# Performance work log

Measured on AMD Instinct MI355X. Metric: run time of the kernel, lower is better.

Reference implementation:

```python
import jax, jax.numpy as jnp
import numpy as np

BS, N, H = 8, 2048, 512
NEG_INF = -1.0e9
LEAKY_SLOPE = 0.01  # torch nn.LeakyReLU default


def setup_inputs() -> dict:
    key = jax.random.key(0)
    ks = jax.random.split(key, 8)
    feats = jax.random.normal(ks[0], (BS, N, H), dtype=jnp.float32)
    # random 0/1 adjacency with self-loops so every row has >=1 neighbor
    adj = jax.random.randint(ks[1], (BS, N, N), 0, 2).astype(jnp.float32)
    adj = jnp.maximum(adj, jnp.eye(N, dtype=jnp.float32)[None])
    s = 1.0 / np.sqrt(H)
    return {
        "feats": feats,
        "adj_mat": adj,
        "fc_w": jax.random.normal(ks[2], (H, H), dtype=jnp.float32) * s,
        "fc_b": jax.random.normal(ks[3], (H,), dtype=jnp.float32) * s,
        "q_w": jax.random.normal(ks[4], (1, H), dtype=jnp.float32) * s,
        "q_b": jax.random.normal(ks[5], (1,), dtype=jnp.float32) * s,
        "k_w": jax.random.normal(ks[6], (1, H), dtype=jnp.float32) * s,
        "k_b": jax.random.normal(ks[7], (1,), dtype=jnp.float32) * s,
    }


def reference(feats, adj_mat, fc_w, fc_b, q_w, q_b, k_w, k_b):
    # feats: [bs, N, H]; torch Linear: x @ W.T + b
    feat_proj = jnp.einsum("bnh,oh->bno", feats, fc_w) + fc_b          # [bs, N, H]
    q = jnp.einsum("bnh,oh->bno", feat_proj, q_w) + q_b                # [bs, N, 1]
    k = jnp.einsum("bnh,oh->bno", feat_proj, k_w) + k_b                # [bs, N, 1]
    logits = q + jnp.swapaxes(k, 2, 1)                                 # [bs, N, N] broadcast add
    masked = logits + (1.0 - adj_mat) * NEG_INF
    masked = jnp.where(masked >= 0, masked, LEAKY_SLOPE * masked)      # LeakyReLU
    atten = jax.nn.softmax(masked, axis=-1)
    # dropout is identity in eval mode
    out = jnp.einsum("bnm,bmh->bnh", atten, feat_proj)
    return out + feats  # residual=True
```

## Files before the change

kernel.cpp:

```cpp
#include <hip/hip_runtime.h>
#include <hip/hip_bf16.h>
#include <cstdint>
#include <cstddef>

#define BSZ 8
#define NN 2048
#define HH 512
#define MROWS (BSZ * NN)
#define LOG2E 1.44269504088896f

typedef __attribute__((ext_vector_type(4))) float f32x4;
typedef __attribute__((ext_vector_type(8))) short short8;
typedef __attribute__((ext_vector_type(4))) unsigned short us4;
typedef __attribute__((ext_vector_type(2))) uint32_t u32x2;

#if __has_builtin(__builtin_amdgcn_exp2f)
#define EXP2(x) __builtin_amdgcn_exp2f(x)
#else
#define EXP2(x) __expf((x) * 0.69314718056f)
#endif

static __device__ __forceinline__ unsigned short f2bf(float f) {
    uint32_t u = __builtin_bit_cast(uint32_t, f);
    u += 0x7fffu + ((u >> 16) & 1u);
    return (unsigned short)(u >> 16);
}

static __device__ __forceinline__ void async16(const unsigned short* g, unsigned short* l) {
    __builtin_amdgcn_global_load_lds(
        (const __attribute__((address_space(1))) void*)g,
        (__attribute__((address_space(3))) void*)l, 16, 0, 0);
}

__global__ __launch_bounds__(256) void prep_kernel(
    const float* __restrict__ feats, const float* __restrict__ fc_w,
    unsigned short* __restrict__ feats_bf, unsigned short* __restrict__ fcw_bf) {
    const int bid = blockIdx.x;
    const int tid = threadIdx.x;
    if (bid < 2048) {
        const int base = bid * 1024 + tid;
#pragma unroll
        for (int j = 0; j < 4; ++j) {
            const int i = base + j * 256;
            f32x4 v = ((const f32x4*)feats)[i];
            us4 o;
#pragma unroll
            for (int c = 0; c < 4; ++c) o[c] = f2bf(v[c]);
            ((us4*)feats_bf)[i] = o;
        }
    } else {
        const int base = (bid - 2048) * 1024 + tid;
#pragma unroll
        for (int j = 0; j < 4; ++j) {
            const int i = base + j * 256;
            f32x4 v = ((const f32x4*)fc_w)[i];
            us4 o;
#pragma unroll
            for (int c = 0; c < 4; ++c) o[c] = f2bf(v[c]);
            ((us4*)fcw_bf)[i] = o;
        }
    }
}

__global__ __launch_bounds__(256) void k2_kernel(
    const unsigned short* __restrict__ A, const unsigned short* __restrict__ Bt,
    const float* __restrict__ fc_b, const float* __restrict__ q_w,
    const float* __restrict__ k_w,
    unsigned short* __restrict__ fpT,
    float* __restrict__ qpart, float* __restrict__ kpart) {
    __shared__ alignas(16) unsigned short As[2][64 * 32];
    __shared__ alignas(16) unsigned short Bs[2][128 * 32];
    __shared__ float qred[2][64], kred[2][64];
    const int bid = blockIdx.x;
    const int tid = threadIdx.x;
    const int wave = tid >> 6, lane = tid & 63;
    const int wi = wave >> 1, wj = wave & 1;
    const int g = bid;
    const int n0 = (g & 3) * 128;
    const int i0 = (g >> 2) * 64;
    const int K = HH;
    const int lrow = lane >> 2;
    const int lseg = (lane & 3) * 8;
    const int fro = (lane & 15) * 32 + (lane >> 4) * 8;
    f32x4 acc[2][4];
#pragma unroll
    for (int a = 0; a < 2; ++a)
#pragma unroll
        for (int c = 0; c < 4; ++c) acc[a][c] = (f32x4)(0.f);

    auto stage = [&](int buf, int k0) {
        const unsigned short* ga = A + (size_t)(i0 + wave * 16 + lrow) * K + k0 + lseg;
        async16(ga, &As[buf][(wave * 16) * 32]);
        const unsigned short* gb = Bt + (size_t)(n0 + wave * 32 + lrow) * K + k0 + lseg;
        async16(gb, &Bs[buf][(wave * 32) * 32]);
        async16(gb + (size_t)16 * K, &Bs[buf][(wave * 32 + 16) * 32]);
    };

    stage(0, 0);
    __syncthreads();

    for (int k0 = 0; k0 < K; k0 += 32) {
        const int p = (k0 >> 5) & 1;
        if (k0 + 32 < K) stage(p ^ 1, k0 + 32);
        short8 af[2], bf[4];
#pragma unroll
        for (int t = 0; t < 2; ++t) af[t] = *(const short8*)&As[p][(wi * 32 + t * 16) * 32 + fro];
#pragma unroll
        for (int t = 0; t < 4; ++t) bf[t] = *(const short8*)&Bs[p][(wj * 64 + t * 16) * 32 + fro];
#pragma unroll
        for (int it = 0; it < 2; ++it)
#pragma unroll
            for (int jt = 0; jt < 4; ++jt)
                acc[it][jt] = __builtin_amdgcn_mfma_f32_16x16x32_bf16(af[it], bf[jt], acc[it][jt], 0, 0, 0);
        __syncthreads();
    }

    int colv[4]; float cbv[4], qwv[4], kwv[4];
#pragma unroll
    for (int jt = 0; jt < 4; ++jt) {
        colv[jt] = n0 + wj * 64 + jt * 16 + (lane & 15);
        cbv[jt] = fc_b[colv[jt]];
        qwv[jt] = q_w[colv[jt]];
        kwv[jt] = k_w[colv[jt]];
    }
    const int b = i0 >> 11;
    const int il = i0 & 2047;
#pragma unroll
    for (int jt = 0; jt < 4; ++jt) {
#pragma unroll
        for (int it = 0; it < 2; ++it) {
            const int rb = wi * 32 + it * 16 + ((lane >> 4) << 2);
            us4 o;
#pragma unroll
            for (int r = 0; r < 4; ++r) o[r] = f2bf(acc[it][jt][r] + cbv[jt]);
            *(us4*)(fpT + ((size_t)b * HH + colv[jt]) * NN + il + rb) = o;
        }
    }
#pragma unroll
    for (int it = 0; it < 2; ++it) {
#pragma unroll
        for (int r = 0; r < 4; ++r) {
            float pq = 0.f, pk = 0.f;
#pragma unroll
            for (int jt = 0; jt < 4; ++jt) {
                float v = acc[it][jt][r] + cbv[jt];
                pq += v * qwv[jt];
                pk += v * kwv[jt];
            }
            for (int off = 1; off < 16; off <<= 1) {
                pq += __shfl_xor(pq, off, 64);
                pk += __shfl_xor(pk, off, 64);
            }
            if ((lane & 15) == 0) {
                const int rr = wi * 32 + it * 16 + ((lane >> 4) << 2) + r;
                qred[wj][rr] = pq;
                kred[wj][rr] = pk;
            }
        }
    }
    __syncthreads();
    if (tid < 64) {
        const size_t o = (size_t)(n0 >> 7) * MROWS + i0 + tid;
        qpart[o] = qred[0][tid] + qred[1][tid];
        kpart[o] = kred[0][tid] + kred[1][tid];
    }
}

__global__ __launch_bounds__(512) void fused_pv_kernel(
    const unsigned short* __restrict__ fpT, const float* __restrict__ adj,
    const float* __restrict__ qpart, const float* __restrict__ kpart,
    const float* __restrict__ q_b, const float* __restrict__ k_b,
    const float* __restrict__ feats, float* __restrict__ out) {
    __shared__ alignas(16) unsigned short As[3][64 * 32];
    __shared__ alignas(16) unsigned short Bs[3][256 * 32];
    __shared__ float kLDS[NN];
    __shared__ float qLDS[64];
    __shared__ float rzl[64];
    const int tid = threadIdx.x;
    const int wave = tid >> 6, lane = tid & 63;
    const int bid = blockIdx.x;
    const int b = bid & 7;
    const int t6 = bid >> 3;
    const int i0 = (t6 >> 1) * 64;
    const int n0 = (t6 & 1) * 256;
    const size_t rowbase = (size_t)b * NN + i0;

    {
        const float kb = k_b[0], qb = q_b[0];
#pragma unroll
        for (int s = 0; s < 4; ++s) {
            const int j = s * 512 + tid;
            const size_t gj = (size_t)b * NN + j;
            kLDS[j] = (kpart[gj] + kpart[MROWS + gj] + kpart[2 * MROWS + gj]
                     + kpart[3 * MROWS + gj] + kb) * LOG2E;
        }
        if (tid < 64) {
            const size_t gi = rowbase + tid;
            qLDS[tid] = (qpart[gi] + qpart[MROWS + gi] + qpart[2 * MROWS + gi]
                       + qpart[3 * MROWS + gi] + qb) * LOG2E;
        }
    }
    __syncthreads();

    const int r0 = tid >> 3;
    const int c4 = (tid & 7) * 4;
    const float qi = qLDS[r0];

    const unsigned short* Bt = fpT + (size_t)b * HH * NN;
    const float* adjRow = adj + (rowbase + r0) * NN + c4;
    const int lrow = lane >> 2, lseg = (lane & 3) * 8;
    const int fro = (lane & 15) * 32 + (lane >> 4) * 8;

    auto stageB = [&](int buf, int k0) {
        const int rbase = wave * 32;
        const unsigned short* gb = Bt + (size_t)(n0 + rbase + lrow) * NN + k0 + lseg;
        async16(gb, &Bs[buf][rbase * 32]);
        async16(gb + (size_t)16 * NN, &Bs[buf][(rbase + 16) * 32]);
    };
    auto transform = [&](int buf, int k0, f32x4 av) {
        const f32x4 kv = *(const f32x4*)&kLDS[k0 + c4];
        float wv[4];
#pragma unroll
        for (int c = 0; c < 4; ++c) {
            float s = qi + kv[c];
            s = fmaxf(s, 0.01f * s);
            const float e = EXP2(s);
            wv[c] = (av[c] != 0.f) ? e : 0.f;
        }
        u32x2 pk;
#pragma unroll
        for (int p = 0; p < 2; ++p) {
            const uint32_t lo = __builtin_bit_cast(uint32_t, wv[2 * p]);
            const uint32_t hi = __builtin_bit_cast(uint32_t, wv[2 * p + 1]);
            pk[p] = __builtin_amdgcn_perm(hi, lo, 0x07060302u);
        }
        *(u32x2*)&As[buf][r0 * 32 + c4] = pk;
    };

    f32x4 acc[4][2];
#pragma unroll
    for (int a = 0; a < 4; ++a)
#pragma unroll
        for (int c = 0; c < 2; ++c) acc[a][c] = (f32x4)(0.f);
    f32x4 acc_z[4] = {(f32x4)(0.f), (f32x4)(0.f), (f32x4)(0.f), (f32x4)(0.f)};
    short8 ones;
#pragma unroll
    for (int j = 0; j < 8; ++j) ones[j] = (short)0x3F80;

    auto compute = [&](int rd) {
        short8 af[4], bf[2];
#pragma unroll
        for (int t = 0; t < 4; ++t) af[t] = *(const short8*)&As[rd][(t * 16) * 32 + fro];
#pragma unroll
        for (int t = 0; t < 2; ++t) bf[t] = *(const short8*)&Bs[rd][(wave * 32 + t * 16) * 32 + fro];
        __builtin_amdgcn_s_setprio(1);
#pragma unroll
        for (int it = 0; it < 4; ++it)
#pragma unroll
            for (int jt = 0; jt < 2; ++jt)
                acc[it][jt] = __builtin_amdgcn_mfma_f32_16x16x32_bf16(af[it], bf[jt], acc[it][jt], 0, 0, 0);
        if (wave == 0) {
#pragma unroll
            for (int it = 0; it < 4; ++it)
                acc_z[it] = __builtin_amdgcn_mfma_f32_16x16x32_bf16(af[it], ones, acc_z[it], 0, 0, 0);
        }
        __builtin_amdgcn_s_setprio(0);
    };

    auto iterbody = [&](int j, int wcnt, f32x4 avUse, f32x4& avLoad) {
        const int st = (j + 1) % 3;
        avLoad = *(const f32x4*)(adjRow + (size_t)(j + 2) * 32);
        stageB(st, (j + 1) * 32);
        if (wcnt == 3) { asm volatile("s_waitcnt vmcnt(3)" ::: "memory"); }
        else          { asm volatile("s_waitcnt vmcnt(4)" ::: "memory"); }
        __builtin_amdgcn_sched_barrier(0);
        transform(st, (j + 1) * 32, avUse);
        asm volatile("s_waitcnt lgkmcnt(0)" ::: "memory");
        __builtin_amdgcn_sched_barrier(0);
        __builtin_amdgcn_s_barrier();
        __builtin_amdgcn_sched_barrier(0);
        compute(j % 3);
    };

    stageB(0, 0);
    f32x4 avA = *(const f32x4*)(adjRow);
    asm volatile("s_waitcnt vmcnt(0)" ::: "memory");
    __builtin_amdgcn_sched_barrier(0);
    transform(0, 0, avA);
    avA = *(const f32x4*)(adjRow + 32);
    asm volatile("s_waitcnt lgkmcnt(0)" ::: "memory");
    __builtin_amdgcn_sched_barrier(0);
    __builtin_amdgcn_s_barrier();
    __builtin_amdgcn_sched_barrier(0);

    f32x4 avB;
    iterbody(0, 4, avA, avB);
    for (int jj = 1; jj < 61; jj += 2) {
        iterbody(jj,     3, avB, avA);
        iterbody(jj + 1, 3, avA, avB);
    }
    iterbody(61, 3, avB, avA);
    {
        const int k0 = 62 * 32;
        stageB(0, k0 + 32);
        asm volatile("s_waitcnt vmcnt(2)" ::: "memory");
        __builtin_amdgcn_sched_barrier(0);
        transform(0, k0 + 32, avA);
        asm volatile("s_waitcnt lgkmcnt(0)" ::: "memory");
        __builtin_amdgcn_sched_barrier(0);
        __builtin_amdgcn_s_barrier();
        __builtin_amdgcn_sched_barrier(0);
        compute(62 % 3);
    }
    {
        asm volatile("s_waitcnt vmcnt(0)" ::: "memory");
        __builtin_amdgcn_sched_barrier(0);
        asm volatile("s_waitcnt lgkmcnt(0)" ::: "memory");
        __builtin_amdgcn_s_barrier();
        __builtin_amdgcn_sched_barrier(0);
        compute(0);
    }

    if (wave == 0 && (lane & 15) == 0) {
#pragma unroll
        for (int it = 0; it < 4; ++it) {
            const int rb = it * 16 + ((lane >> 4) << 2);
#pragma unroll
            for (int r = 0; r < 4; ++r) rzl[rb + r] = 1.0f / acc_z[it][r];
        }
    }
    __syncthreads();

#pragma unroll
    for (int it = 0; it < 4; ++it) {
        const int rb = it * 16 + ((lane >> 4) << 2);
        float rv[4];
#pragma unroll
        for (int r = 0; r < 4; ++r) rv[r] = rzl[rb + r];
#pragma unroll
        for (int jt = 0; jt < 2; ++jt) {
            const int col = n0 + wave * 32 + jt * 16 + (lane & 15);
#pragma unroll
            for (int r = 0; r < 4; ++r) {
                const size_t idx = (rowbase + rb + r) * HH + col;
                out[idx] = acc[it][jt][r] * rv[r] + feats[idx];
            }
        }
    }
}

extern "C" void kernel_launch(void* const* d_in, const int* in_sizes, int n_in,
                              void* d_out, int out_size, void* d_ws, size_t ws_size,
                              hipStream_t stream) {
    const float* feats = (const float*)d_in[0];
    const float* adj   = (const float*)d_in[1];
    const float* fc_w  = (const float*)d_in[2];
    const float* fc_b  = (const float*)d_in[3];
    const float* q_w   = (const float*)d_in[4];
    const float* q_b   = (const float*)d_in[5];
    const float* k_w   = (const float*)d_in[6];
    const float* k_b   = (const float*)d_in[7];
    float* out = (float*)d_out;

    char* w = (char*)d_ws;
    auto alloc = [&](size_t bytes) {
        char* p = w;
        w += (bytes + 255) & ~(size_t)255;
        return p;
    };
    unsigned short* feats_bf = (unsigned short*)alloc((size_t)BSZ * NN * HH * 2);
    unsigned short* fcw_bf   = (unsigned short*)alloc((size_t)HH * HH * 2);
    unsigned short* fpT   = (unsigned short*)alloc((size_t)BSZ * HH * NN * 2);
    float* qpart = (float*)alloc((size_t)4 * MROWS * 4);
    float* kpart = (float*)alloc((size_t)4 * MROWS * 4);

    prep_kernel<<<2112, 256, 0, stream>>>(feats, fc_w, feats_bf, fcw_bf);
    k2_kernel<<<1024, 256, 0, stream>>>(feats_bf, fcw_bf, fc_b, q_w, k_w,
                                        fpT, qpart, kpart);
    fused_pv_kernel<<<512, 512, 0, stream>>>(
        fpT, adj, qpart, kpart, q_b, k_b, feats, out);
}
```

Baseline: 322.9 us.

## Load B fragments directly from global into registers, dropping LDS staging

The B operand (transposed projected features) is no longer copied asynchronously into a triple-buffered LDS tile. Each wave now loads its MFMA B fragments straight from global memory into registers, one step ahead, through a register double buffer. This frees most of the shared memory and removes the LDS round trip and its vmcnt waits. In exchange, the global loads are uncoalesced 16-byte row-strided reads, and their latency is now hidden only by the compiler's waits, so stalls may increase.

After: 339.9 us. 5.3% more time.

```diff
diff --git a/kernel.cpp b/kernel.cpp
--- a/kernel.cpp
+++ b/kernel.cpp
@@ -172,7 +172,6 @@
     const float* __restrict__ q_b, const float* __restrict__ k_b,
     const float* __restrict__ feats, float* __restrict__ out) {
     __shared__ alignas(16) unsigned short As[3][64 * 32];
-    __shared__ alignas(16) unsigned short Bs[3][256 * 32];
     __shared__ float kLDS[NN];
     __shared__ float qLDS[64];
     __shared__ float rzl[64];
@@ -206,16 +205,14 @@
     const int c4 = (tid & 7) * 4;
     const float qi = qLDS[r0];
 
-    const unsigned short* Bt = fpT + (size_t)b * HH * NN;
     const float* adjRow = adj + (rowbase + r0) * NN + c4;
-    const int lrow = lane >> 2, lseg = (lane & 3) * 8;
+    const unsigned short* bfBase =
+        fpT + ((size_t)b * HH + n0 + wave * 32 + (lane & 15)) * NN + (lane >> 4) * 8;
     const int fro = (lane & 15) * 32 + (lane >> 4) * 8;
 
-    auto stageB = [&](int buf, int k0) {
-        const int rbase = wave * 32;
-        const unsigned short* gb = Bt + (size_t)(n0 + rbase + lrow) * NN + k0 + lseg;
-        async16(gb, &Bs[buf][rbase * 32]);
-        async16(gb + (size_t)16 * NN, &Bs[buf][(rbase + 16) * 32]);
+    auto loadBF = [&](int t, short8& b0, short8& b1) {
+        b0 = *(const short8*)(bfBase + (size_t)t * 32);
+        b1 = *(const short8*)(bfBase + (size_t)16 * NN + (size_t)t * 32);
     };
     auto transform = [&](int buf, int k0, f32x4 av) {
         const f32x4 kv = *(const f32x4*)&kLDS[k0 + c4];
@@ -247,18 +244,16 @@
 #pragma unroll
     for (int j = 0; j < 8; ++j) ones[j] = (short)0x3F80;
 
-    auto compute = [&](int rd) {
-        short8 af[4], bf[2];
+    auto compute = [&](int rd, short8 b0, short8 b1) {
+        short8 af[4];
 #pragma unroll
         for (int t = 0; t < 4; ++t) af[t] = *(const short8*)&As[rd][(t * 16) * 32 + fro];
-#pragma unroll
-        for (int t = 0; t < 2; ++t) bf[t] = *(const short8*)&Bs[rd][(wave * 32 + t * 16) * 32 + fro];
         __builtin_amdgcn_s_setprio(1);
 #pragma unroll
-        for (int it = 0; it < 4; ++it)
-#pragma unroll
-            for (int jt = 0; jt < 2; ++jt)
-                acc[it][jt] = __builtin_amdgcn_mfma_f32_16x16x32_bf16(af[it], bf[jt], acc[it][jt], 0, 0, 0);
+        for (int it = 0; it < 4; ++it) {
+            acc[it][0] = __builtin_amdgcn_mfma_f32_16x16x32_bf16(af[it], b0, acc[it][0], 0, 0, 0);
+            acc[it][1] = __builtin_amdgcn_mfma_f32_16x16x32_bf16(af[it], b1, acc[it][1], 0, 0, 0);
+        }
         if (wave == 0) {
 #pragma unroll
             for (int it = 0; it < 4; ++it)
@@ -267,59 +262,43 @@
         __builtin_amdgcn_s_setprio(0);
     };
 
-    auto iterbody = [&](int j, int wcnt, f32x4 avUse, f32x4& avLoad) {
-        const int st = (j + 1) % 3;
+    auto iterbody = [&](int j, f32x4 avUse, f32x4& avLoad,
+                        short8 bU0, short8 bU1, short8& bL0, short8& bL1) {
         avLoad = *(const f32x4*)(adjRow + (size_t)(j + 2) * 32);
-        stageB(st, (j + 1) * 32);
-        if (wcnt == 3) { asm volatile("s_waitcnt vmcnt(3)" ::: "memory"); }
-        else          { asm volatile("s_waitcnt vmcnt(4)" ::: "memory"); }
-        __builtin_amdgcn_sched_barrier(0);
-        transform(st, (j + 1) * 32, avUse);
+        loadBF(j + 1, bL0, bL1);
+        transform((j + 1) % 3, (j + 1) * 32, avUse);
         asm volatile("s_waitcnt lgkmcnt(0)" ::: "memory");
         __builtin_amdgcn_sched_barrier(0);
         __builtin_amdgcn_s_barrier();
         __builtin_amdgcn_sched_barrier(0);
-        compute(j % 3);
-    };
-
-    stageB(0, 0);
+        compute(j % 3, bU0, bU1);
+    };
+
     f32x4 avA = *(const f32x4*)(adjRow);
-    asm volatile("s_waitcnt vmcnt(0)" ::: "memory");
-    __builtin_amdgcn_sched_barrier(0);
+    f32x4 avB;
     transform(0, 0, avA);
     avA = *(const f32x4*)(adjRow + 32);
+    short8 bA0, bA1, bB0, bB1;
+    loadBF(0, bA0, bA1);
     asm volatile("s_waitcnt lgkmcnt(0)" ::: "memory");
     __builtin_amdgcn_sched_barrier(0);
     __builtin_amdgcn_s_barrier();
     __builtin_amdgcn_sched_barrier(0);
 
-    f32x4 avB;
-    iterbody(0, 4, avA, avB);
-    for (int jj = 1; jj < 61; jj += 2) {
-        iterbody(jj,     3, avB, avA);
-        iterbody(jj + 1, 3, avA, avB);
-    }
-    iterbody(61, 3, avB, avA);
+    for (int jj = 0; jj < 62; jj += 2) {
+        iterbody(jj,     avA, avB, bA0, bA1, bB0, bB1);
+        iterbody(jj + 1, avB, avA, bB0, bB1, bA0, bA1);
+    }
     {
-        const int k0 = 62 * 32;
-        stageB(0, k0 + 32);
-        asm volatile("s_waitcnt vmcnt(2)" ::: "memory");
-        __builtin_amdgcn_sched_barrier(0);
-        transform(0, k0 + 32, avA);
+        loadBF(63, bB0, bB1);
+        transform(0, 63 * 32, avA);
         asm volatile("s_waitcnt lgkmcnt(0)" ::: "memory");
         __builtin_amdgcn_sched_barrier(0);
         __builtin_amdgcn_s_barrier();
         __builtin_amdgcn_sched_barrier(0);
-        compute(62 % 3);
-    }
-    {
-        asm volatile("s_waitcnt vmcnt(0)" ::: "memory");
-        __builtin_amdgcn_sched_barrier(0);
-        asm volatile("s_waitcnt lgkmcnt(0)" ::: "memory");
-        __builtin_amdgcn_s_barrier();
-        __builtin_amdgcn_sched_barrier(0);
-        compute(0);
-    }
+        compute(2, bA0, bA1);
+    }
+    compute(0, bB0, bB1);
 
     if (wave == 0 && (lane & 15) == 0) {
 #pragma unroll
```
